# Kernel optimization log

Measured on AMD Instinct MI355X. Metric: run time of the kernel, lower is better.

Reference implementation:

```python
import jax, jax.numpy as jnp
import numpy as np

N = 32768          # tokens per modal
TOKEN_DIM = 1024
HID_DIM = 1024
SENSE_DIM = 256
K = 512            # centroids (shared size across modals)


def setup_inputs() -> dict:
    key = jax.random.key(0)
    ks = jax.random.split(key, 10)
    s = 0.02
    return {
        "text_emb": jax.random.normal(ks[0], (N, TOKEN_DIM), jnp.float32),
        "image_emb": jax.random.normal(ks[1], (N, TOKEN_DIM), jnp.float32),
        "text_W1": jax.random.normal(ks[2], (TOKEN_DIM, HID_DIM), jnp.float32) * s,
        "text_W2": jax.random.normal(ks[3], (HID_DIM, HID_DIM), jnp.float32) * s,
        "text_W3": jax.random.normal(ks[4], (HID_DIM, SENSE_DIM), jnp.float32) * s,
        "image_W1": jax.random.normal(ks[5], (TOKEN_DIM, HID_DIM), jnp.float32) * s,
        "image_W2": jax.random.normal(ks[6], (HID_DIM, HID_DIM), jnp.float32) * s,
        "image_W3": jax.random.normal(ks[7], (HID_DIM, SENSE_DIM), jnp.float32) * s,
        "centroids_raw": jax.random.uniform(ks[8], (K, SENSE_DIM), jnp.float32),
    }


def _sense_map(x, W1, W2, W3):
    # Linear(bias=False)+Tanh x3
    h = jnp.tanh(x @ W1)
    h = jnp.tanh(h @ W2)
    return jnp.tanh(h @ W3)  # [N, sense_dim]


def _assign(se, centroids):
    # squared distance [K, N] via expansion (same math as broadcast-subtract)
    c2 = jnp.sum(centroids * centroids, axis=1)[:, None]      # [K,1]
    e2 = jnp.sum(se * se, axis=1)[None, :]                     # [1,N]
    sqdist = c2 + e2 - 2.0 * (centroids @ se.T)                # [K,N]
    # torch argmax over (sqdist.T == min) picks first min -> argmin first occurrence
    return jnp.argmin(sqdist, axis=0)                          # [N] int


def reference(text_emb, image_emb, text_W1, text_W2, text_W3,
              image_W1, image_W2, image_W3, centroids_raw):
    centroids = jnp.tanh(centroids_raw)
    se_t = _sense_map(text_emb, text_W1, text_W2, text_W3)
    se_i = _sense_map(image_emb, image_W1, image_W2, image_W3)
    sc_t = _assign(se_t, centroids)
    sc_i = _assign(se_i, centroids)

    sense_embeddings = jnp.concatenate([se_t, se_i], axis=0)   # [2N, sense_dim]
    sense_class = jnp.concatenate([sc_t, sc_i], axis=0)        # [2N]
    word_class = jnp.concatenate([jnp.zeros((N,), jnp.int32),
                                  jnp.ones((N,), jnp.int32)])

    # ragged per-sense grouping represented jit-compatibly as a stable sort
    # permutation + per-sense counts (per modal)
    order_t = jnp.argsort(sc_t, stable=True)
    order_i = jnp.argsort(sc_i, stable=True)
    counts_t = jnp.zeros((K,), jnp.int32).at[sc_t].add(1)
    counts_i = jnp.zeros((K,), jnp.int32).at[sc_i].add(1)

    return (centroids, sense_embeddings, word_class, sense_class,
            order_t, counts_t, order_i, counts_i)
```

## Files before the change

### kernel.cpp

```cpp
#include <hip/hip_runtime.h>
#include <math.h>

#define NTOK 32768
typedef unsigned short ushort_t;

#define OFF_CENT 0
#define OFF_SE   131072
#define OFF_WC   16908288
#define OFF_SC   16973824
#define OFF_OT   17039360
#define OFF_CT   17072128
#define OFF_OI   17072640
#define OFF_CI   17105408

typedef __attribute__((ext_vector_type(8))) short short8v;
typedef __attribute__((ext_vector_type(4))) float f32x4;

__device__ __forceinline__ float dot4(float4 a, float4 b){
    return a.x*b.x + a.y*b.y + a.z*b.z + a.w*b.w;
}

__device__ __forceinline__ ushort_t f2bf(float x){
    unsigned int u = __float_as_uint(x);
    unsigned int r = (u + 0x7fffu + ((u >> 16) & 1u)) >> 16;
    return (ushort_t)r;
}
__device__ __forceinline__ float bf2f(ushort_t h){
    return __uint_as_float(((unsigned int)h) << 16);
}

__device__ __forceinline__ void gload16(const void* g, void* l){
    __builtin_amdgcn_global_load_lds(
        (const __attribute__((address_space(1))) void*)g,
        (__attribute__((address_space(3))) void*)l,
        16, 0, 0);
}

__device__ __forceinline__ void cvt8(float4 a, float4 b, short8v& h, short8v& l){
    float x[8] = {a.x, a.y, a.z, a.w, b.x, b.y, b.z, b.w};
    #pragma unroll
    for (int i = 0; i < 8; ++i) {
        ushort_t hh = f2bf(x[i]);
        h[i] = (short)hh;
        l[i] = (short)f2bf(x[i] - bf2f(hh));
    }
}

__global__ __launch_bounds__(64) void k_cent(const float* __restrict__ raw,
                                             float* __restrict__ out,
                                             float* __restrict__ c2,
                                             ushort_t* __restrict__ ch,
                                             ushort_t* __restrict__ cl)
{
    int c = blockIdx.x, l = threadIdx.x;
    float4 v = *(const float4*)(raw + (size_t)c*256 + l*4);
    float4 t;
    t.x = tanhf(v.x); t.y = tanhf(v.y); t.z = tanhf(v.z); t.w = tanhf(v.w);
    *(float4*)(out + OFF_CENT + (size_t)c*256 + l*4) = t;
    ushort4 h = make_ushort4(f2bf(t.x), f2bf(t.y), f2bf(t.z), f2bf(t.w));
    ushort4 lo = make_ushort4(f2bf(t.x - bf2f(h.x)), f2bf(t.y - bf2f(h.y)),
                              f2bf(t.z - bf2f(h.z)), f2bf(t.w - bf2f(h.w)));
    *(ushort4*)(ch + (size_t)c*256 + l*4) = h;
    *(ushort4*)(cl + (size_t)c*256 + l*4) = lo;
    float s = dot4(t, t);
    #pragma unroll
    for (int off = 32; off > 0; off >>= 1) s += __shfl_down(s, off);
    if (l == 0) c2[c] = s;
}

__global__ __launch_bounds__(256) void k_esplit(const float* __restrict__ x,
                                                ushort_t* __restrict__ hi,
                                                ushort_t* __restrict__ lo,
                                                long n4)
{
    long g = (long)blockIdx.x*256 + threadIdx.x;
    if (g >= n4) return;
    float4 v = ((const float4*)x)[g];
    ushort_t h0 = f2bf(v.x), h1 = f2bf(v.y), h2 = f2bf(v.z), h3 = f2bf(v.w);
    ushort4 h = make_ushort4(h0, h1, h2, h3);
    ushort4 l = make_ushort4(f2bf(v.x - bf2f(h0)), f2bf(v.y - bf2f(h1)),
                             f2bf(v.z - bf2f(h2)), f2bf(v.w - bf2f(h3)));
    ((ushort4*)hi)[g] = h;
    ((ushort4*)lo)[g] = l;
}

__device__ __forceinline__ void wsplit_tile(const float* __restrict__ W,
                                            ushort_t* __restrict__ Wt_hi,
                                            ushort_t* __restrict__ Wt_lo,
                                            int K, int N, int bx, int by)
{
    __shared__ float t[32][33];
    int k0 = by*32, n0 = bx*32;
    int tx = threadIdx.x & 31, ty = threadIdx.x >> 5;
    #pragma unroll
    for (int r = 0; r < 4; ++r)
        t[ty + r*8][tx] = W[(size_t)(k0 + ty + r*8)*N + n0 + tx];
    __syncthreads();
    #pragma unroll
    for (int r = 0; r < 4; ++r) {
        int n = ty + r*8;
        float x = t[tx][n];
        ushort_t h = f2bf(x);
        Wt_hi[(size_t)(n0+n)*K + k0 + tx] = h;
        Wt_lo[(size_t)(n0+n)*K + k0 + tx] = f2bf(x - bf2f(h));
    }
}

__global__ __launch_bounds__(256) void k_prep(
    const float* __restrict__ W1t, const float* __restrict__ W2t, const float* __restrict__ W3t,
    const float* __restrict__ W1i, const float* __restrict__ W2i, const float* __restrict__ W3i,
    ushort_t* __restrict__ wreg, float* __restrict__ out)
{
    const size_t WM = 4*1048576 + 2*262144;
    int b = blockIdx.x;
    if (b >= 4608) {
        int g = (b - 4608)*256 + threadIdx.x;
        float v = (g*4 < NTOK) ? 0.f : 1.f;
        ((float4*)(out + OFF_WC))[g] = make_float4(v, v, v, v);
        return;
    }
    int m = b / 2304;
    int r = b % 2304;
    ushort_t* base = wreg + (size_t)m*WM;
    const float* Ws[3][2] = {{W1t, W1i}, {W2t, W2i}, {W3t, W3i}};
    if (r < 1024) {
        wsplit_tile(Ws[0][m], base, base + 1048576, 1024, 1024, r % 32, r / 32);
    } else if (r < 2048) {
        int r2 = r - 1024;
        wsplit_tile(Ws[1][m], base + 2*1048576, base + 3*1048576, 1024, 1024, r2 % 32, r2 / 32);
    } else {
        int r3 = r - 2048;
        wsplit_tile(Ws[2][m], base + 4*1048576, base + 4*1048576 + 262144, 1024, 256, r3 % 8, r3 / 8);
    }
}

__global__ __launch_bounds__(512, 2) void k_gemm_l1(
    const float* __restrict__ Af, const ushort_t* __restrict__ Bt_hi,
    ushort_t* __restrict__ C_hi, ushort_t* __restrict__ C_lo,
    unsigned bDelta, int N)
{
    __shared__ ushort_t lds[65536];

    const int tid  = threadIdx.x;
    const int wave = tid >> 6, lane = tid & 63;
    const int wr = wave >> 2, wc = wave & 3;
    const int fr = lane & 15, fq = lane >> 4;

    int nwg = gridDim.x;
    int id = blockIdx.x;
    if (!(nwg & 7)) { int cpx = nwg >> 3; id = (id & 7)*cpx + (id >> 3); }
    const int nx = N >> 8;
    const int n0 = (id % nx) * 256;
    const int m0 = (id / nx) * 256;

    const int srow0 = tid >> 2;
    const int qx = (tid & 3) ^ ((srow0 >> 1) & 3);

    const float* fA0 = Af + (size_t)(m0 + srow0) * 1024 + qx*8;
    const float* fA1 = fA0 + 131072;
    const unsigned offB0 = (unsigned)(n0 + srow0) * 1024u + (unsigned)qx * 8u;
    const ushort_t* pB0  = Bt_hi + offB0;
    const ushort_t* pB1  = pB0 + 131072u;
    const ushort_t* pB0l = pB0 + bDelta;
    const ushort_t* pB1l = pB1 + bDelta;
    const unsigned ldsS0 = (unsigned)wave * 512u;
    const unsigned ldsS1 = ldsS0 + 4096u;
    const unsigned wOff  = ldsS0 + (unsigned)lane * 8u;

    const unsigned fb = (unsigned)fr*32u + (unsigned)((fq ^ ((fr >> 1) & 3)) * 8);
    const ushort_t* p0 = lds + fb;
    const ushort_t* p1 = p0 + 32768u;

    f32x4 acc[8][4] = {};

#define STGB(KT, WB) { \
    unsigned wb_ = (unsigned)(WB) * 32768u; \
    gload16(pB0  + (KT), lds + wb_ + 16384u + ldsS0); \
    gload16(pB1  + (KT), lds + wb_ + 16384u + ldsS1); \
    gload16(pB0l + (KT), lds + wb_ + 24576u + ldsS0); \
    gload16(pB1l + (KT), lds + wb_ + 24576u + ldsS1); \
}
#define RA1(P, hl, i) (*(const short8v*)((P) + (hl)*8192u + (unsigned)wr*4096u + (unsigned)(i)*512u))
#define RB1(P, hl, j) (*(const short8v*)((P) + 16384u + (hl)*8192u + (unsigned)wc*2048u + (unsigned)(j)*512u))
#define MM16(A8, B8, C4) __builtin_amdgcn_mfma_f32_16x16x32_bf16(A8, B8, C4, 0, 0, 0)

    {
        float4 a00 = *(const float4*)(fA0);
        float4 a01 = *(const float4*)(fA0 + 4);
        float4 a10 = *(const float4*)(fA1);
        float4 a11 = *(const float4*)(fA1 + 4);
        STGB(0, 0);
        short8v h0, l0, h1, l1;
        cvt8(a00, a01, h0, l0);
        cvt8(a10, a11, h1, l1);
        *(short8v*)(lds + wOff)          = h0;
        *(short8v*)(lds + 4096u + wOff)  = h1;
        *(short8v*)(lds + 8192u + wOff)  = l0;
        *(short8v*)(lds + 12288u + wOff) = l1;
    }
    __syncthreads();

    #pragma unroll 1
    for (int kt = 0; kt < 1024; kt += 32) {
        const int par = (kt >> 5) & 1;
        const ushort_t* cp = par ? p1 : p0;
        const bool pf = (kt + 32) < 1024;

        float4 a00, a01, a10, a11;
        if (pf) {
            a00 = *(const float4*)(fA0 + kt + 32);
            a01 = *(const float4*)(fA0 + kt + 36);
            a10 = *(const float4*)(fA1 + kt + 32);
            a11 = *(const float4*)(fA1 + kt + 36);
            STGB(kt + 32, par ^ 1);
        }

        short8v bh0 = RB1(cp,0,0), bl0 = RB1(cp,1,0);
        short8v bh1 = RB1(cp,0,1), bl1 = RB1(cp,1,1);
        short8v bh2 = RB1(cp,0,2), bl2 = RB1(cp,1,2);
        short8v bh3 = RB1(cp,0,3), bl3 = RB1(cp,1,3);

        __builtin_amdgcn_s_setprio(1);
        #pragma unroll
        for (int i = 0; i < 8; ++i) {
            short8v ah = RA1(cp,0,i), al = RA1(cp,1,i);
            acc[i][0] = MM16(ah, bh0, acc[i][0]);
            acc[i][1] = MM16(ah, bh1, acc[i][1]);
            acc[i][2] = MM16(ah, bh2, acc[i][2]);
            acc[i][3] = MM16(ah, bh3, acc[i][3]);
            acc[i][0] = MM16(ah, bl0, acc[i][0]);
            acc[i][1] = MM16(ah, bl1, acc[i][1]);
            acc[i][2] = MM16(ah, bl2, acc[i][2]);
            acc[i][3] = MM16(ah, bl3, acc[i][3]);
            acc[i][0] = MM16(al, bh0, acc[i][0]);
            acc[i][1] = MM16(al, bh1, acc[i][1]);
            acc[i][2] = MM16(al, bh2, acc[i][2]);
            acc[i][3] = MM16(al, bh3, acc[i][3]);
        }
        __builtin_amdgcn_s_setprio(0);

        if (pf) {
            unsigned wb = (unsigned)(par ^ 1) * 32768u;
            short8v h0, l0, h1, l1;
            cvt8(a00, a01, h0, l0);
            cvt8(a10, a11, h1, l1);
            *(short8v*)(lds + wb + wOff)          = h0;
            *(short8v*)(lds + wb + 4096u + wOff)  = h1;
            *(short8v*)(lds + wb + 8192u + wOff)  = l0;
            *(short8v*)(lds + wb + 12288u + wOff) = l1;
        }
        __syncthreads();
    }

    #pragma unroll
    for (int i = 0; i < 8; ++i)
        #pragma unroll
        for (int j = 0; j < 4; ++j)
            #pragma unroll
            for (int r = 0; r < 4; ++r) {
                int row = m0 + wr*128 + i*16 + fq*4 + r;
                int col = n0 + wc*64 + j*16 + fr;
                float t = tanhf(acc[i][j][r]);
                size_t idx = (size_t)row*N + col;
                ushort_t h = f2bf(t);
                C_hi[idx] = h;
                C_lo[idx] = f2bf(t - bf2f(h));
            }
#undef STGB
#undef RA1
#undef RB1
#undef MM16
}

__global__ __launch_bounds__(512, 2) void k_gemm_mfma256(
    const ushort_t* __restrict__ A_hi, const ushort_t* __restrict__ Bt_hi,
    ushort_t* __restrict__ C_hi, ushort_t* __restrict__ C_lo,
    unsigned aDelta, unsigned bDelta, int N)
{
    __shared__ ushort_t lds[65536];

    const int tid  = threadIdx.x;
    const int wave = tid >> 6, lane = tid & 63;
    const int wr = wave >> 2, wc = wave & 3;
    const int fr = lane & 15, fq = lane >> 4;

    int nwg = gridDim.x;
    int id = blockIdx.x;
    if (!(nwg & 7)) { int cpx = nwg >> 3; id = (id & 7)*cpx + (id >> 3); }
    const int nx = N >> 8;
    const int n0 = (id % nx) * 256;
    const int m0 = (id / nx) * 256;

    const int srow0 = tid >> 2;
    const int qx = (tid & 3) ^ ((srow0 >> 1) & 3);

    const unsigned offA0 = (unsigned)(m0 + srow0) * 1024u + (unsigned)qx * 8u;
    const unsigned offB0 = (unsigned)(n0 + srow0) * 1024u + (unsigned)qx * 8u;
    const ushort_t* pA0  = A_hi + offA0;
    const ushort_t* pA1  = pA0 + 131072u;
    const ushort_t* pA0l = pA0 + aDelta;
    const ushort_t* pA1l = pA1 + aDelta;
    const ushort_t* pB0  = Bt_hi + offB0;
    const ushort_t* pB1  = pB0 + 131072u;
    const ushort_t* pB0l = pB0 + bDelta;
    const ushort_t* pB1l = pB1 + bDelta;
    const unsigned ldsS0 = (unsigned)wave * 512u;
    const unsigned ldsS1 = ldsS0 + 4096u;

    const unsigned fb = (unsigned)fr*32u + (unsigned)((fq ^ ((fr >> 1) & 3)) * 8);
    const ushort_t* p0 = lds + fb;
    const ushort_t* p1 = p0 + 32768u;

    f32x4 acc[8][4] = {};

#define STG(KT, WB) { \
    unsigned wb_ = (unsigned)(WB) * 32768u; \
    gload16(pA0  + (KT), lds + wb_ +           ldsS0); \
    gload16(pA1  + (KT), lds + wb_ +           ldsS1); \
    gload16(pA0l + (KT), lds + wb_ +  8192u +  ldsS0); \
    gload16(pA1l + (KT), lds + wb_ +  8192u +  ldsS1); \
    gload16(pB0  + (KT), lds + wb_ + 16384u +  ldsS0); \
    gload16(pB1  + (KT), lds + wb_ + 16384u +  ldsS1); \
    gload16(pB0l + (KT), lds + wb_ + 24576u +  ldsS0); \
    gload16(pB1l + (KT), lds + wb_ + 24576u +  ldsS1); \
}
#define RA(P, hl, i) (*(const short8v*)((P) + (hl)*8192u + (unsigned)wr*4096u + (unsigned)(i)*512u))
#define RB(P, hl, j) (*(const short8v*)((P) + 16384u + (hl)*8192u + (unsigned)wc*2048u + (unsigned)(j)*512u))
#define MM16(A8, B8, C4) __builtin_amdgcn_mfma_f32_16x16x32_bf16(A8, B8, C4, 0, 0, 0)

    STG(0, 0);
    __syncthreads();

    #pragma unroll 1
    for (int kt = 0; kt < 1024; kt += 32) {
        const int par = (kt >> 5) & 1;
        const ushort_t* cp = par ? p1 : p0;

        short8v bh0 = RB(cp,0,0), bl0 = RB(cp,1,0);
        short8v bh1 = RB(cp,0,1), bl1 = RB(cp,1,1);
        short8v bh2 = RB(cp,0,2), bl2 = RB(cp,1,2);
        short8v bh3 = RB(cp,0,3), bl3 = RB(cp,1,3);

        if (kt + 32 < 1024) STG(kt + 32, par ^ 1);

        __builtin_amdgcn_s_setprio(1);
        #pragma unroll
        for (int i = 0; i < 8; ++i) {
            short8v ah = RA(cp,0,i), al = RA(cp,1,i);
            acc[i][0] = MM16(ah, bh0, acc[i][0]);
            acc[i][1] = MM16(ah, bh1, acc[i][1]);
            acc[i][2] = MM16(ah, bh2, acc[i][2]);
            acc[i][3] = MM16(ah, bh3, acc[i][3]);
            acc[i][0] = MM16(ah, bl0, acc[i][0]);
            acc[i][1] = MM16(ah, bl1, acc[i][1]);
            acc[i][2] = MM16(ah, bl2, acc[i][2]);
            acc[i][3] = MM16(ah, bl3, acc[i][3]);
            acc[i][0] = MM16(al, bh0, acc[i][0]);
            acc[i][1] = MM16(al, bh1, acc[i][1]);
            acc[i][2] = MM16(al, bh2, acc[i][2]);
            acc[i][3] = MM16(al, bh3, acc[i][3]);
        }
        __builtin_amdgcn_s_setprio(0);

        __syncthreads();
    }

    #pragma unroll
    for (int i = 0; i < 8; ++i)
        #pragma unroll
        for (int j = 0; j < 4; ++j)
            #pragma unroll
            for (int r = 0; r < 4; ++r) {
                int row = m0 + wr*128 + i*16 + fq*4 + r;
                int col = n0 + wc*64 + j*16 + fr;
                float t = tanhf(acc[i][j][r]);
                size_t idx = (size_t)row*N + col;
                ushort_t h = f2bf(t);
                C_hi[idx] = h;
                C_lo[idx] = f2bf(t - bf2f(h));
            }
#undef STG
#undef RA
#undef RB
#undef MM16
}

__global__ __launch_bounds__(256, 2) void k_gemm_mfma(
    const ushort_t* __restrict__ A_hi, const ushort_t* __restrict__ A_lo,
    const ushort_t* __restrict__ Bt_hi, const ushort_t* __restrict__ Bt_lo,
    ushort_t* __restrict__ C_hi, ushort_t* __restrict__ C_lo,
    float* __restrict__ Cf,
    int N)
{
    const int K = 1024;
    __shared__ ushort_t lds[16384];

    const int tid  = threadIdx.x;
    const int wave = tid >> 6, lane = tid & 63;
    const int wr = wave >> 1, wc = wave & 1;

    int nwg = gridDim.x * gridDim.y;
    int id = blockIdx.y * gridDim.x + blockIdx.x;
    if (!(nwg & 7)) { int cpx = nwg >> 3; id = (id & 7)*cpx + (id >> 3); }
    const int m0 = (id / gridDim.x) * 128, n0 = (id % gridDim.x) * 128;

    f32x4 acc[4][4] = {};

    int srow[2], sq[2], slbase[2];
    #pragma unroll
    for (int r = 0; r < 2; ++r) {
        int row = wave*32 + r*16 + (lane >> 2);
        srow[r]   = row;
        sq[r]     = (lane & 3) ^ ((row >> 1) & 3);
        slbase[r] = wave*1024 + r*512;
    }

    const int fr = lane & 15, fq = lane >> 4;

    for (int kt = 0; kt < K; kt += 32) {
        __syncthreads();
        #pragma unroll
        for (int r = 0; r < 2; ++r) {
            size_t ga = (size_t)(m0 + srow[r]) * K + kt + sq[r]*8;
            size_t gb = (size_t)(n0 + srow[r]) * K + kt + sq[r]*8;
            gload16(A_hi  + ga, lds          + slbase[r]);
            gload16(A_lo  + ga, lds + 4096   + slbase[r]);
            gload16(Bt_hi + gb, lds + 8192   + slbase[r]);
            gload16(Bt_lo + gb, lds + 12288  + slbase[r]);
        }
        __syncthreads();

        short8v ah[4], al[4], bh[4], bl[4];
        #pragma unroll
        for (int i = 0; i < 4; ++i) {
            int rowa = wr*64 + i*16 + fr;
            int offa = rowa*32 + ((fq ^ ((rowa >> 1) & 3)) * 8);
            ah[i] = *(const short8v*)(lds + offa);
            al[i] = *(const short8v*)(lds + 4096 + offa);
            int rowb = wc*64 + i*16 + fr;
            int offb = rowb*32 + ((fq ^ ((rowb >> 1) & 3)) * 8);
            bh[i] = *(const short8v*)(lds + 8192 + offb);
            bl[i] = *(const short8v*)(lds + 12288 + offb);
        }
        #pragma unroll
        for (int i = 0; i < 4; ++i)
            #pragma unroll
            for (int j = 0; j < 4; ++j) {
                acc[i][j] = __builtin_amdgcn_mfma_f32_16x16x32_bf16(ah[i], bh[j], acc[i][j], 0, 0, 0);
                acc[i][j] = __builtin_amdgcn_mfma_f32_16x16x32_bf16(ah[i], bl[j], acc[i][j], 0, 0, 0);
                acc[i][j] = __builtin_amdgcn_mfma_f32_16x16x32_bf16(al[i], bh[j], acc[i][j], 0, 0, 0);
            }
    }

    #pragma unroll
    for (int i = 0; i < 4; ++i)
        #pragma unroll
        for (int j = 0; j < 4; ++j)
            #pragma unroll
            for (int r = 0; r < 4; ++r) {
                int row = m0 + wr*64 + i*16 + fq*4 + r;
                int col = n0 + wc*64 + j*16 + fr;
                float t = tanhf(acc[i][j][r]);
                size_t idx = (size_t)row*N + col;
                if (Cf) Cf[idx] = t;
                if (C_hi) {
                    ushort_t h = f2bf(t);
                    C_hi[idx] = h;
                    C_lo[idx] = f2bf(t - bf2f(h));
                }
            }
}

__global__ __launch_bounds__(256) void k_assign_mfma(
    const ushort_t* __restrict__ SEh, const ushort_t* __restrict__ SEl,
    const ushort_t* __restrict__ ch, const ushort_t* __restrict__ cl,
    const float* __restrict__ c2,
    int* __restrict__ sc, float* __restrict__ out_w,
    int* __restrict__ blockHist)
{
    __shared__ ushort_t lds[16384];
    __shared__ float c2s[512];
    __shared__ float redD[128][2];
    __shared__ int   redI[128][2];

    const int modal = blockIdx.y;
    const int t0 = blockIdx.x * 128;
    const int tid  = threadIdx.x;
    const int wave = tid >> 6, lane = tid & 63;
    const int wr = wave >> 1, wc = wave & 1;
    const int fr = lane & 15, fq = lane >> 4;

    const ushort_t* seh = SEh + (size_t)modal * NTOK * 256;
    const ushort_t* sel = SEl + (size_t)modal * NTOK * 256;

    c2s[tid] = c2[tid];
    c2s[tid + 256] = c2[tid + 256];

    int srow[2], sq[2], slbase[2];
    #pragma unroll
    for (int r = 0; r < 2; ++r) {
        int row = wave*32 + r*16 + (lane >> 2);
        srow[r]   = row;
        sq[r]     = (lane & 3) ^ ((row >> 1) & 3);
        slbase[r] = wave*1024 + r*512;
    }

    float bd[16]; int bi[16];
    #pragma unroll
    for (int s = 0; s < 16; ++s) { bd[s] = 3.4e38f; bi[s] = 0; }

    for (int j = 0; j < 4; ++j) {
        f32x4 acc[4][4] = {};
        for (int kt = 0; kt < 256; kt += 32) {
            __syncthreads();
            #pragma unroll
            for (int r = 0; r < 2; ++r) {
                size_t ga = (size_t)(t0 + srow[r]) * 256 + kt + sq[r]*8;
                size_t gc = (size_t)(j*128 + srow[r]) * 256 + kt + sq[r]*8;
                gload16(seh + ga, lds          + slbase[r]);
                gload16(sel + ga, lds + 4096   + slbase[r]);
                gload16(ch  + gc, lds + 8192   + slbase[r]);
                gload16(cl  + gc, lds + 12288  + slbase[r]);
            }
// ... 208 lines not shown
    }
    classBase[modal*512 + c] = s[c] - total;
}

__global__ __launch_bounds__(256) void k_scatter(const int* __restrict__ sc,
                                                 const int* __restrict__ blockBase,
                                                 const int* __restrict__ classBase,
                                                 float* __restrict__ out)
{
    int modal = blockIdx.y, blk = blockIdx.x, tid = threadIdx.x;
    __shared__ int cls[256];
    int t = blk*256 + tid;
    int c = sc[modal*NTOK + t];
    cls[tid] = c;
    __syncthreads();
    int rank = 0;
    for (int j = 0; j < tid; ++j) rank += (cls[j] == c) ? 1 : 0;
    int pos = classBase[modal*512 + c] + blockBase[(modal*128 + blk)*512 + c] + rank;
    float* oo = out + (modal ? OFF_OI : OFF_OT);
    oo[pos] = (float)t;
}

extern "C" void kernel_launch(void* const* d_in, const int* in_sizes, int n_in,
                              void* d_out, int out_size, void* d_ws, size_t ws_size,
                              hipStream_t stream)
{
    const float* text_emb  = (const float*)d_in[0];
    const float* image_emb = (const float*)d_in[1];
    const float* W[2][3] = {
        {(const float*)d_in[2], (const float*)d_in[3], (const float*)d_in[4]},
        {(const float*)d_in[5], (const float*)d_in[6], (const float*)d_in[7]}
    };
    const float* cent_raw = (const float*)d_in[8];
    float* out = (float*)d_out;
    char* w = (char*)d_ws;

    int*   sc        = (int*)w;
    int*   blockHist = (int*)(w + 0x40000);
    int*   blockBase = (int*)(w + 0xC0000);
    int*   classBase = (int*)(w + 0x140000);
    float* c2        = (float*)(w + 0x141000);
    ushort_t* cent_h = (ushort_t*)(w + 0x142000);
    ushort_t* cent_l = (ushort_t*)(w + 0x182000);

    ushort_t* wreg = (ushort_t*)(w + 0x200000);
    const size_t WM = 4*1048576 + 2*262144;

    ushort_t* SEh = (ushort_t*)(w + 0x1400000);
    ushort_t* SEl = (ushort_t*)(w + 0x3400000);

    bool mfmaAssign = true;
    size_t actoff = 0x5400000;
    int Mc = 0;
    for (int c = NTOK; c >= 128; c >>= 1)
        if (actoff + (size_t)c*8192 <= ws_size) { Mc = c; break; }
    if (Mc == 0) {
        mfmaAssign = false;
        actoff = 0x1400000;
        for (int c = NTOK; c >= 128; c >>= 1)
            if (actoff + (size_t)c*8192 <= ws_size) { Mc = c; break; }
        if (Mc == 0) Mc = 128;
    }
    ushort_t* act = (ushort_t*)(w + actoff);
    const bool big = (Mc % 256 == 0);

    hipMemsetAsync(blockHist, 0, 2*128*512*sizeof(int), stream);

    k_cent<<<dim3(512), dim3(64), 0, stream>>>(cent_raw, out, c2, cent_h, cent_l);
    k_prep<<<dim3(4672), dim3(256), 0, stream>>>(
        W[0][0], W[0][1], W[0][2], W[1][0], W[1][1], W[1][2], wreg, out);

    for (int m = 0; m < 2; ++m) {
        const float* emb = m ? image_emb : text_emb;
        ushort_t* w1h = wreg + (size_t)m*WM;
        ushort_t* w1l = w1h + 1048576;
        ushort_t* w2h = w1l + 1048576;
        ushort_t* w2l = w2h + 1048576;
        ushort_t* w3h = w2l + 1048576;
        ushort_t* w3l = w3h + 262144;

        ushort_t* Ah = act;
        ushort_t* Al = Ah + (size_t)Mc*1024;
        ushort_t* Hh = Al + (size_t)Mc*1024;
        ushort_t* Hl = Hh + (size_t)Mc*1024;

        for (int s0 = 0; s0 < NTOK; s0 += Mc) {
            if (big) {
                k_gemm_l1<<<dim3((Mc/256)*4), dim3(512), 0, stream>>>(
                    emb + (size_t)s0*1024, w1h, Hh, Hl, 1048576u, 1024);
                k_gemm_mfma256<<<dim3((Mc/256)*4), dim3(512), 0, stream>>>(
                    Hh, w2h, Ah, Al, (unsigned)Mc*1024u, 1048576u, 1024);
            } else {
                long n4 = (long)Mc*1024/4;
                k_esplit<<<dim3((unsigned)((n4 + 255)/256)), dim3(256), 0, stream>>>(
                    emb + (size_t)s0*1024, Ah, Al, n4);
                k_gemm_mfma<<<dim3(8, Mc/128), dim3(256), 0, stream>>>(
                    Ah, Al, w1h, w1l, Hh, Hl, nullptr, 1024);
                k_gemm_mfma<<<dim3(8, Mc/128), dim3(256), 0, stream>>>(
                    Hh, Hl, w2h, w2l, Ah, Al, nullptr, 1024);
            }
            ushort_t* seh_ptr = mfmaAssign ? SEh + ((size_t)m*NTOK + s0)*256 : nullptr;
            ushort_t* sel_ptr = mfmaAssign ? SEl + ((size_t)m*NTOK + s0)*256 : nullptr;
            k_gemm_mfma<<<dim3(2, Mc/128), dim3(256), 0, stream>>>(
                Ah, Al, w3h, w3l, seh_ptr, sel_ptr,
                out + OFF_SE + ((size_t)m*NTOK + s0)*256, 256);
        }
    }

    if (mfmaAssign) {
        k_assign_mfma<<<dim3(256, 2), dim3(256), 0, stream>>>(
            SEh, SEl, cent_h, cent_l, c2, sc, out, blockHist);
    } else {
        k_assign<<<dim3(512, 2), dim3(256), 0, stream>>>(out, c2, sc, out, blockHist);
    }
    k_scan   <<<dim3(2),      dim3(512), 0, stream>>>(blockHist, blockBase, classBase, out);
    k_scatter<<<dim3(128, 2), dim3(256), 0, stream>>>(sc, blockBase, classBase, out);
}
```

Measured before the change: 1.042 ms.

## Use 32x32x16 MFMA with plane-blocked weight and hidden layouts for layers 1-2

Switches the two big GEMM kernels from 16x16x32 to 32x32x16 bf16 MFMA and stores the W1/W2 weights and the layer-1 output in a k-plane-blocked layout. Global-to-LDS copies become contiguous and match the fragment reads without XOR swizzling. The fallback path for chunk sizes below 256 is removed. The aim is fewer LDS reads per MFMA and cheaper addressing. The risk is more LDS bank conflicts from the unswizzled reads and scattered output stores in the layer-1 epilogue.

```diff
diff --git a/kernel.cpp b/kernel.cpp
--- a/kernel.cpp
+++ b/kernel.cpp
@@ -15,6 +15,11 @@
 
 typedef __attribute__((ext_vector_type(8))) short short8v;
 typedef __attribute__((ext_vector_type(4))) float f32x4;
+typedef __attribute__((ext_vector_type(16))) float f32x16;
+
+#define PLANE 2048
+#define KTBLK 8192
+#define RBLK  262144
 
 __device__ __forceinline__ float dot4(float4 a, float4 b){
     return a.x*b.x + a.y*b.y + a.z*b.z + a.w*b.w;
@@ -68,26 +73,36 @@
     if (l == 0) c2[c] = s;
 }
 
-__global__ __launch_bounds__(256) void k_esplit(const float* __restrict__ x,
-                                                ushort_t* __restrict__ hi,
-                                                ushort_t* __restrict__ lo,
-                                                long n4)
-{
-    long g = (long)blockIdx.x*256 + threadIdx.x;
-    if (g >= n4) return;
-    float4 v = ((const float4*)x)[g];
-    ushort_t h0 = f2bf(v.x), h1 = f2bf(v.y), h2 = f2bf(v.z), h3 = f2bf(v.w);
-    ushort4 h = make_ushort4(h0, h1, h2, h3);
-    ushort4 l = make_ushort4(f2bf(v.x - bf2f(h0)), f2bf(v.y - bf2f(h1)),
-                             f2bf(v.z - bf2f(h2)), f2bf(v.w - bf2f(h3)));
-    ((ushort4*)hi)[g] = h;
-    ((ushort4*)lo)[g] = l;
-}
-
-__device__ __forceinline__ void wsplit_tile(const float* __restrict__ W,
-                                            ushort_t* __restrict__ Wt_hi,
-                                            ushort_t* __restrict__ Wt_lo,
-                                            int K, int N, int bx, int by)
+__device__ __forceinline__ void wsplit_plane(const float* __restrict__ W,
+                                             ushort_t* __restrict__ Wt_hi,
+                                             ushort_t* __restrict__ Wt_lo,
+                                             int N, int bx, int by)
+{
+    __shared__ float t[32][33];
+    int k0 = by*32, n0 = bx*32;
+    int tx = threadIdx.x & 31, ty = threadIdx.x >> 5;
+    #pragma unroll
+    for (int r = 0; r < 4; ++r)
+        t[ty + r*8][tx] = W[(size_t)(k0 + ty + r*8)*N + n0 + tx];
+    __syncthreads();
+    const int kt = k0 >> 5;
+    const int s  = tx >> 3, e = tx & 7;
+    #pragma unroll
+    for (int r = 0; r < 4; ++r) {
+        int nl = ty + r*8;
+        int n = n0 + nl;
+        float x = t[tx][nl];
+        ushort_t h = f2bf(x);
+        size_t dst = (size_t)(n >> 8)*RBLK + (size_t)kt*KTBLK + s*PLANE + (n & 255)*8 + e;
+        Wt_hi[dst] = h;
+        Wt_lo[dst] = f2bf(x - bf2f(h));
+    }
+}
+
+__device__ __forceinline__ void wsplit_plain(const float* __restrict__ W,
+                                             ushort_t* __restrict__ Wt_hi,
+                                             ushort_t* __restrict__ Wt_lo,
+                                             int K, int N, int bx, int by)
 {
     __shared__ float t[32][33];
     int k0 = by*32, n0 = bx*32;
@@ -124,86 +139,114 @@
     ushort_t* base = wreg + (size_t)m*WM;
     const float* Ws[3][2] = {{W1t, W1i}, {W2t, W2i}, {W3t, W3i}};
     if (r < 1024) {
-        wsplit_tile(Ws[0][m], base, base + 1048576, 1024, 1024, r % 32, r / 32);
+        wsplit_plane(Ws[0][m], base, base + 1048576, 1024, r % 32, r / 32);
     } else if (r < 2048) {
         int r2 = r - 1024;
-        wsplit_tile(Ws[1][m], base + 2*1048576, base + 3*1048576, 1024, 1024, r2 % 32, r2 / 32);
+        wsplit_plane(Ws[1][m], base + 2*1048576, base + 3*1048576, 1024, r2 % 32, r2 / 32);
     } else {
         int r3 = r - 2048;
-        wsplit_tile(Ws[2][m], base + 4*1048576, base + 4*1048576 + 262144, 1024, 256, r3 % 8, r3 / 8);
-    }
+        wsplit_plain(Ws[2][m], base + 4*1048576, base + 4*1048576 + 262144, 1024, 256, r3 % 8, r3 / 8);
+    }
+}
+
+#define MM32(A8, B8, C16) __builtin_amdgcn_mfma_f32_32x32x16_bf16(A8, B8, C16, 0, 0, 0)
+
+#define RAP(P, hl, kk, i) (*(const short8v*)((P) + (hl)*8192u + (kk)*4096u + (unsigned)(i)*256u))
+#define RBP(P, hl, kk, j) (*(const short8v*)((P) + 16384u + (hl)*8192u + (kk)*4096u + (unsigned)(j)*256u))
+
+#define MFMA_TILE(PA, PB) { \
+    short8v b000 = RBP(PB,0,0,0), b001 = RBP(PB,1,0,0); \
+    short8v b010 = RBP(PB,0,1,0), b011 = RBP(PB,1,1,0); \
+    short8v b100 = RBP(PB,0,0,1), b101 = RBP(PB,1,0,1); \
+    short8v b110 = RBP(PB,0,1,1), b111 = RBP(PB,1,1,1); \
+    __builtin_amdgcn_s_setprio(1); \
+    _Pragma("unroll") \
+    for (int i = 0; i < 4; ++i) { \
+        short8v ah0 = RAP(PA,0,0,i), al0 = RAP(PA,1,0,i); \
+        short8v ah1 = RAP(PA,0,1,i), al1 = RAP(PA,1,1,i); \
+        acc[i][0] = MM32(ah0, b000, acc[i][0]); \
+        acc[i][1] = MM32(ah0, b100, acc[i][1]); \
+        acc[i][0] = MM32(ah0, b001, acc[i][0]); \
+        acc[i][1] = MM32(ah0, b101, acc[i][1]); \
+        acc[i][0] = MM32(al0, b000, acc[i][0]); \
+        acc[i][1] = MM32(al0, b100, acc[i][1]); \
+        acc[i][0] = MM32(ah1, b010, acc[i][0]); \
+        acc[i][1] = MM32(ah1, b110, acc[i][1]); \
+        acc[i][0] = MM32(ah1, b011, acc[i][0]); \
+        acc[i][1] = MM32(ah1, b111, acc[i][1]); \
+        acc[i][0] = MM32(al1, b010, acc[i][0]); \
+        acc[i][1] = MM32(al1, b110, acc[i][1]); \
+    } \
+    __builtin_amdgcn_s_setprio(0); \
 }
 
 __global__ __launch_bounds__(512, 2) void k_gemm_l1(
-    const float* __restrict__ Af, const ushort_t* __restrict__ Bt_hi,
+    const float* __restrict__ Af, const ushort_t* __restrict__ Btp,
     ushort_t* __restrict__ C_hi, ushort_t* __restrict__ C_lo,
-    unsigned bDelta, int N)
+    unsigned bDelta)
 {
     __shared__ ushort_t lds[65536];
 
     const int tid  = threadIdx.x;
     const int wave = tid >> 6, lane = tid & 63;
     const int wr = wave >> 2, wc = wave & 3;
-    const int fr = lane & 15, fq = lane >> 4;
+    const int l31 = lane & 31, lk = lane >> 5;
 
     int nwg = gridDim.x;
     int id = blockIdx.x;
     if (!(nwg & 7)) { int cpx = nwg >> 3; id = (id & 7)*cpx + (id >> 3); }
-    const int nx = N >> 8;
-    const int n0 = (id % nx) * 256;
-    const int m0 = (id / nx) * 256;
-
-    const int srow0 = tid >> 2;
-    const int qx = (tid & 3) ^ ((srow0 >> 1) & 3);
-
-    const float* fA0 = Af + (size_t)(m0 + srow0) * 1024 + qx*8;
+    const int n0 = (id & 3) * 256;
+    const int m0 = (id >> 2) * 256;
+
+    const int q  = tid & 3;
+    const int sr = tid >> 2;
+    const float* fA0 = Af + (size_t)(m0 + sr) * 1024 + q*8;
     const float* fA1 = fA0 + 131072;
-    const unsigned offB0 = (unsigned)(n0 + srow0) * 1024u + (unsigned)qx * 8u;
-    const ushort_t* pB0  = Bt_hi + offB0;
-    const ushort_t* pB1  = pB0 + 131072u;
+    const unsigned aw0 = (unsigned)q*PLANE + (unsigned)sr*8u;
+    const unsigned aw1 = aw0 + 1024u;
+
+    const ushort_t* pB0 = Btp + (size_t)(n0 >> 8)*RBLK + wave*512 + lane*8;
     const ushort_t* pB0l = pB0 + bDelta;
-    const ushort_t* pB1l = pB1 + bDelta;
-    const unsigned ldsS0 = (unsigned)wave * 512u;
-    const unsigned ldsS1 = ldsS0 + 4096u;
-    const unsigned wOff  = ldsS0 + (unsigned)lane * 8u;
-
-    const unsigned fb = (unsigned)fr*32u + (unsigned)((fq ^ ((fr >> 1) & 3)) * 8);
-    const ushort_t* p0 = lds + fb;
-    const ushort_t* p1 = p0 + 32768u;
-
-    f32x4 acc[8][4] = {};
-
-#define STGB(KT, WB) { \
+    const unsigned ldsB0 = 16384u + (unsigned)wave*512u;
+
+    const unsigned fbu = (unsigned)lk*PLANE + (unsigned)l31*8u;
+    const ushort_t* pA = lds + fbu + (unsigned)wr*1024u;
+    const ushort_t* pB = lds + fbu + (unsigned)wc*512u;
+    const ushort_t* pA1b = pA + 32768u;
+    const ushort_t* pB1b = pB + 32768u;
+
+    f32x16 acc[4][2] = {};
+
+#define STGB1(KT, WB) { \
     unsigned wb_ = (unsigned)(WB) * 32768u; \
-    gload16(pB0  + (KT), lds + wb_ + 16384u + ldsS0); \
-    gload16(pB1  + (KT), lds + wb_ + 16384u + ldsS1); \
-    gload16(pB0l + (KT), lds + wb_ + 24576u + ldsS0); \
-    gload16(pB1l + (KT), lds + wb_ + 24576u + ldsS1); \
-}
-#define RA1(P, hl, i) (*(const short8v*)((P) + (hl)*8192u + (unsigned)wr*4096u + (unsigned)(i)*512u))
-#define RB1(P, hl, j) (*(const short8v*)((P) + 16384u + (hl)*8192u + (unsigned)wc*2048u + (unsigned)(j)*512u))
-#define MM16(A8, B8, C4) __builtin_amdgcn_mfma_f32_16x16x32_bf16(A8, B8, C4, 0, 0, 0)
+    unsigned ko = (unsigned)(KT) * 256u; \
+    gload16(pB0  + ko,        lds + wb_ + ldsB0); \
+    gload16(pB0  + ko + 4096, lds + wb_ + ldsB0 + 4096u); \
+    gload16(pB0l + ko,        lds + wb_ + 8192u + ldsB0); \
+    gload16(pB0l + ko + 4096, lds + wb_ + 8192u + ldsB0 + 4096u); \
+}
 
     {
         float4 a00 = *(const float4*)(fA0);
         float4 a01 = *(const float4*)(fA0 + 4);
         float4 a10 = *(const float4*)(fA1);
         float4 a11 = *(const float4*)(fA1 + 4);
-        STGB(0, 0);
+        STGB1(0, 0);
         short8v h0, l0, h1, l1;
         cvt8(a00, a01, h0, l0);
         cvt8(a10, a11, h1, l1);
-        *(short8v*)(lds + wOff)          = h0;
-        *(short8v*)(lds + 4096u + wOff)  = h1;
-        *(short8v*)(lds + 8192u + wOff)  = l0;
-        *(short8v*)(lds + 12288u + wOff) = l1;
+        *(short8v*)(lds + aw0)          = h0;
+        *(short8v*)(lds + aw1)          = h1;
+        *(short8v*)(lds + 8192u + aw0)  = l0;
+        *(short8v*)(lds + 8192u + aw1)  = l1;
     }
     __syncthreads();
 
     #pragma unroll 1
     for (int kt = 0; kt < 1024; kt += 32) {
         const int par = (kt >> 5) & 1;
-        const ushort_t* cp = par ? p1 : p0;
+        const ushort_t* cpA = par ? pA1b : pA;
+        const ushort_t* cpB = par ? pB1b : pB;
         const bool pf = (kt + 32) < 1024;
 
         float4 a00, a01, a10, a11;
@@ -212,177 +255,119 @@
             a01 = *(const float4*)(fA0 + kt + 36);
             a10 = *(const float4*)(fA1 + kt + 32);
             a11 = *(const float4*)(fA1 + kt + 36);
-            STGB(kt + 32, par ^ 1);
-        }
-
-        short8v bh0 = RB1(cp,0,0), bl0 = RB1(cp,1,0);
-        short8v bh1 = RB1(cp,0,1), bl1 = RB1(cp,1,1);
-        short8v bh2 = RB1(cp,0,2), bl2 = RB1(cp,1,2);
-        short8v bh3 = RB1(cp,0,3), bl3 = RB1(cp,1,3);
-
-        __builtin_amdgcn_s_setprio(1);
-        #pragma unroll
-        for (int i = 0; i < 8; ++i) {
-            short8v ah = RA1(cp,0,i), al = RA1(cp,1,i);
-            acc[i][0] = MM16(ah, bh0, acc[i][0]);
-            acc[i][1] = MM16(ah, bh1, acc[i][1]);
-            acc[i][2] = MM16(ah, bh2, acc[i][2]);
-            acc[i][3] = MM16(ah, bh3, acc[i][3]);
-            acc[i][0] = MM16(ah, bl0, acc[i][0]);
-            acc[i][1] = MM16(ah, bl1, acc[i][1]);
-            acc[i][2] = MM16(ah, bl2, acc[i][2]);
-            acc[i][3] = MM16(ah, bl3, acc[i][3]);
-            acc[i][0] = MM16(al, bh0, acc[i][0]);
-            acc[i][1] = MM16(al, bh1, acc[i][1]);
-            acc[i][2] = MM16(al, bh2, acc[i][2]);
-            acc[i][3] = MM16(al, bh3, acc[i][3]);
-        }
-        __builtin_amdgcn_s_setprio(0);
+            STGB1(kt + 32, par ^ 1);
+        }
+
+        MFMA_TILE(cpA, cpB)
 
         if (pf) {
             unsigned wb = (unsigned)(par ^ 1) * 32768u;
             short8v h0, l0, h1, l1;
             cvt8(a00, a01, h0, l0);
             cvt8(a10, a11, h1, l1);
-            *(short8v*)(lds + wb + wOff)          = h0;
-            *(short8v*)(lds + wb + 4096u + wOff)  = h1;
-            *(short8v*)(lds + wb + 8192u + wOff)  = l0;
-            *(short8v*)(lds + wb + 12288u + wOff) = l1;
+            *(short8v*)(lds + wb + aw0)          = h0;
+            *(short8v*)(lds + wb + aw1)          = h1;
+            *(short8v*)(lds + wb + 8192u + aw0)  = l0;
+            *(short8v*)(lds + wb + 8192u + aw1)  = l1;
         }
         __syncthreads();
     }
 
     #pragma unroll
-    for (int i = 0; i < 8; ++i)
-        #pragma unroll
-        for (int j = 0; j < 4; ++j)
-            #pragma unroll
-            for (int r = 0; r < 4; ++r) {
-                int row = m0 + wr*128 + i*16 + fq*4 + r;
-                int col = n0 + wc*64 + j*16 + fr;
+    for (int i = 0; i < 4; ++i)
+        #pragma unroll
+        for (int j = 0; j < 2; ++j)
+            #pragma unroll
+            for (int r = 0; r < 16; ++r) {
+                int row = m0 + wr*128 + i*32 + (r & 3) + 8*(r >> 2) + 4*lk;
+                int col = n0 + wc*64 + j*32 + l31;
                 float t = tanhf(acc[i][j][r]);
-                size_t idx = (size_t)row*N + col;
+                size_t idx = (size_t)(row >> 8)*RBLK + (size_t)(col >> 5)*KTBLK
+                           + ((col >> 3) & 3)*PLANE + (row & 255)*8 + (col & 7);
                 ushort_t h = f2bf(t);
                 C_hi[idx] = h;
                 C_lo[idx] = f2bf(t - bf2f(h));
             }
-#undef STGB
-#undef RA1
-#undef RB1
-#undef MM16
-}
-
-__global__ __launch_bounds__(512, 2) void k_gemm_mfma256(
-    const ushort_t* __restrict__ A_hi, const ushort_t* __restrict__ Bt_hi,
+#undef STGB1
+}
+
+__global__ __launch_bounds__(512, 2) void k_gemm_l2(
+    const ushort_t* __restrict__ Ap, const ushort_t* __restrict__ Btp,
     ushort_t* __restrict__ C_hi, ushort_t* __restrict__ C_lo,
-    unsigned aDelta, unsigned bDelta, int N)
+    unsigned aDelta, unsigned bDelta)
 {
     __shared__ ushort_t lds[65536];
 
     const int tid  = threadIdx.x;
     const int wave = tid >> 6, lane = tid & 63;
     const int wr = wave >> 2, wc = wave & 3;
-    const int fr = lane & 15, fq = lane >> 4;
+    const int l31 = lane & 31, lk = lane >> 5;
 
     int nwg = gridDim.x;
     int id = blockIdx.x;
     if (!(nwg & 7)) { int cpx = nwg >> 3; id = (id & 7)*cpx + (id >> 3); }
-    const int nx = N >> 8;
-    const int n0 = (id % nx) * 256;
-    const int m0 = (id / nx) * 256;
-
-    const int srow0 = tid >> 2;
-    const int qx = (tid & 3) ^ ((srow0 >> 1) & 3);
-
-    const unsigned offA0 = (unsigned)(m0 + srow0) * 1024u + (unsigned)qx * 8u;
-    const unsigned offB0 = (unsigned)(n0 + srow0) * 1024u + (unsigned)qx * 8u;
-    const ushort_t* pA0  = A_hi + offA0;
-    const ushort_t* pA1  = pA0 + 131072u;
+    const int n0 = (id & 3) * 256;
+    const int m0 = (id >> 2) * 256;
+
+    const ushort_t* pA0 = Ap  + (size_t)(m0 >> 8)*RBLK + wave*512 + lane*8;
     const ushort_t* pA0l = pA0 + aDelta;
-    const ushort_t* pA1l = pA1 + aDelta;
-    const ushort_t* pB0  = Bt_hi + offB0;
-    const ushort_t* pB1  = pB0 + 131072u;
+    const ushort_t* pB0 = Btp + (size_t)(n0 >> 8)*RBLK + wave*512 + lane*8;
     const ushort_t* pB0l = pB0 + bDelta;
-    const ushort_t* pB1l = pB1 + bDelta;
-    const unsigned ldsS0 = (unsigned)wave * 512u;
-    const unsigned ldsS1 = ldsS0 + 4096u;
-
-    const unsigned fb = (unsigned)fr*32u + (unsigned)((fq ^ ((fr >> 1) & 3)) * 8);
-    const ushort_t* p0 = lds + fb;
-    const ushort_t* p1 = p0 + 32768u;
-
-    f32x4 acc[8][4] = {};
-
-#define STG(KT, WB) { \
+    const unsigned ldsA0 = (unsigned)wave*512u;
+    const unsigned ldsB0 = 16384u + (unsigned)wave*512u;
+
+    const unsigned fbu = (unsigned)lk*PLANE + (unsigned)l31*8u;
+    const ushort_t* pA = lds + fbu + (unsigned)wr*1024u;
+    const ushort_t* pB = lds + fbu + (unsigned)wc*512u;
+    const ushort_t* pA1b = pA + 32768u;
+    const ushort_t* pB1b = pB + 32768u;
+
+    f32x16 acc[4][2] = {};
+
+#define STG2(KT, WB) { \
     unsigned wb_ = (unsigned)(WB) * 32768u; \
-    gload16(pA0  + (KT), lds + wb_ +           ldsS0); \
-    gload16(pA1  + (KT), lds + wb_ +           ldsS1); \
-    gload16(pA0l + (KT), lds + wb_ +  8192u +  ldsS0); \
-    gload16(pA1l + (KT), lds + wb_ +  8192u +  ldsS1); \
-    gload16(pB0  + (KT), lds + wb_ + 16384u +  ldsS0); \
-    gload16(pB1  + (KT), lds + wb_ + 16384u +  ldsS1); \
-    gload16(pB0l + (KT), lds + wb_ + 24576u +  ldsS0); \
-    gload16(pB1l + (KT), lds + wb_ + 24576u +  ldsS1); \
-}
-#define RA(P, hl, i) (*(const short8v*)((P) + (hl)*8192u + (unsigned)wr*4096u + (unsigned)(i)*512u))
-#define RB(P, hl, j) (*(const short8v*)((P) + 16384u + (hl)*8192u + (unsigned)wc*2048u + (unsigned)(j)*512u))
-#define MM16(A8, B8, C4) __builtin_amdgcn_mfma_f32_16x16x32_bf16(A8, B8, C4, 0, 0, 0)
-
-    STG(0, 0);
+    unsigned ko = (unsigned)(KT) * 256u; \
+    gload16(pA0  + ko,        lds + wb_ + ldsA0); \
+    gload16(pA0  + ko + 4096, lds + wb_ + ldsA0 + 4096u); \
+    gload16(pA0l + ko,        lds + wb_ + 8192u + ldsA0); \
+    gload16(pA0l + ko + 4096, lds + wb_ + 8192u + ldsA0 + 4096u); \
+    gload16(pB0  + ko,        lds + wb_ + ldsB0); \
+    gload16(pB0  + ko + 4096, lds + wb_ + ldsB0 + 4096u); \
+    gload16(pB0l + ko,        lds + wb_ + 8192u + ldsB0); \
+    gload16(pB0l + ko + 4096, lds + wb_ + 8192u + ldsB0 + 4096u); \
+}
+
+    STG2(0, 0);
     __syncthreads();
 
     #pragma unroll 1
     for (int kt = 0; kt < 1024; kt += 32) {
         const int par = (kt >> 5) & 1;
-        const ushort_t* cp = par ? p1 : p0;
-
-        short8v bh0 = RB(cp,0,0), bl0 = RB(cp,1,0);
-        short8v bh1 = RB(cp,0,1), bl1 = RB(cp,1,1);
-        short8v bh2 = RB(cp,0,2), bl2 = RB(cp,1,2);
-        short8v bh3 = RB(cp,0,3), bl3 = RB(cp,1,3);
-
-        if (kt + 32 < 1024) STG(kt + 32, par ^ 1);
-
-        __builtin_amdgcn_s_setprio(1);
-        #pragma unroll
-        for (int i = 0; i < 8; ++i) {
-            short8v ah = RA(cp,0,i), al = RA(cp,1,i);
-            acc[i][0] = MM16(ah, bh0, acc[i][0]);
-            acc[i][1] = MM16(ah, bh1, acc[i][1]);
-            acc[i][2] = MM16(ah, bh2, acc[i][2]);
-            acc[i][3] = MM16(ah, bh3, acc[i][3]);
-            acc[i][0] = MM16(ah, bl0, acc[i][0]);
-            acc[i][1] = MM16(ah, bl1, acc[i][1]);
-            acc[i][2] = MM16(ah, bl2, acc[i][2]);
-            acc[i][3] = MM16(ah, bl3, acc[i][3]);
-            acc[i][0] = MM16(al, bh0, acc[i][0]);
-            acc[i][1] = MM16(al, bh1, acc[i][1]);
-            acc[i][2] = MM16(al, bh2, acc[i][2]);
-            acc[i][3] = MM16(al, bh3, acc[i][3]);
-        }
-        __builtin_amdgcn_s_setprio(0);
+        const ushort_t* cpA = par ? pA1b : pA;
+        const ushort_t* cpB = par ? pB1b : pB;
+
+        if (kt + 32 < 1024) STG2(kt + 32, par ^ 1);
+
+        MFMA_TILE(cpA, cpB)
 
         __syncthreads();
     }
 
     #pragma unroll
-    for (int i = 0; i < 8; ++i)
-        #pragma unroll
-        for (int j = 0; j < 4; ++j)
-            #pragma unroll
-            for (int r = 0; r < 4; ++r) {
-                int row = m0 + wr*128 + i*16 + fq*4 + r;
-                int col = n0 + wc*64 + j*16 + fr;
+    for (int i = 0; i < 4; ++i)
+        #pragma unroll
+        for (int j = 0; j < 2; ++j)
+            #pragma unroll
+            for (int r = 0; r < 16; ++r) {
+                int row = m0 + wr*128 + i*32 + (r & 3) + 8*(r >> 2) + 4*lk;
+                int col = n0 + wc*64 + j*32 + l31;
                 float t = tanhf(acc[i][j][r]);
-                size_t idx = (size_t)row*N + col;
+                size_t idx = (size_t)row*1024 + col;
                 ushort_t h = f2bf(t);
                 C_hi[idx] = h;
                 C_lo[idx] = f2bf(t - bf2f(h));
             }
-#undef STG
-#undef RA
-#undef RB
-#undef MM16
+#undef STG2
 }
 
 __global__ __launch_bounds__(256, 2) void k_gemm_mfma(
@@ -783,17 +768,16 @@
     bool mfmaAssign = true;
     size_t actoff = 0x5400000;
     int Mc = 0;
-    for (int c = NTOK; c >= 128; c >>= 1)
+    for (int c = NTOK; c >= 256; c >>= 1)
         if (actoff + (size_t)c*8192 <= ws_size) { Mc = c; break; }
     if (Mc == 0) {
         mfmaAssign = false;
         actoff = 0x1400000;
-        for (int c = NTOK; c >= 128; c >>= 1)
+        for (int c = NTOK; c >= 256; c >>= 1)
             if (actoff + (size_t)c*8192 <= ws_size) { Mc = c; break; }
-        if (Mc == 0) Mc = 128;
+        if (Mc == 0) Mc = 256;
     }
     ushort_t* act = (ushort_t*)(w + actoff);
-    const bool big = (Mc % 256 == 0);
 
     hipMemsetAsync(blockHist, 0, 2*128*512*sizeof(int), stream);
 
@@ -804,10 +788,8 @@
     for (int m = 0; m < 2; ++m) {
         const float* emb = m ? image_emb : text_emb;
         ushort_t* w1h = wreg + (size_t)m*WM;
-        ushort_t* w1l = w1h + 1048576;
-        ushort_t* w2h = w1l + 1048576;
-        ushort_t* w2l = w2h + 1048576;
-        ushort_t* w3h = w2l + 1048576;
+        ushort_t* w2h = w1h + 2*1048576;
+        ushort_t* w3h = w1h + 4*1048576;
         ushort_t* w3l = w3h + 262144;
 
         ushort_t* Ah = act;
@@ -816,20 +798,10 @@
         ushort_t* Hl = Hh + (size_t)Mc*1024;
 
         for (int s0 = 0; s0 < NTOK; s0 += Mc) {
-            if (big) {
-                k_gemm_l1<<<dim3((Mc/256)*4), dim3(512), 0, stream>>>(
-                    emb + (size_t)s0*1024, w1h, Hh, Hl, 1048576u, 1024);
-                k_gemm_mfma256<<<dim3((Mc/256)*4), dim3(512), 0, stream>>>(
-                    Hh, w2h, Ah, Al, (unsigned)Mc*1024u, 1048576u, 1024);
-            } else {
-                long n4 = (long)Mc*1024/4;
-                k_esplit<<<dim3((unsigned)((n4 + 255)/256)), dim3(256), 0, stream>>>(
-                    emb + (size_t)s0*1024, Ah, Al, n4);
-                k_gemm_mfma<<<dim3(8, Mc/128), dim3(256), 0, stream>>>(
-                    Ah, Al, w1h, w1l, Hh, Hl, nullptr, 1024);
-                k_gemm_mfma<<<dim3(8, Mc/128), dim3(256), 0, stream>>>(
-                    Hh, Hl, w2h, w2l, Ah, Al, nullptr, 1024);
-            }
+            k_gemm_l1<<<dim3((Mc/256)*4), dim3(512), 0, stream>>>(
+                emb + (size_t)s0*1024, w1h, Hh, Hl, 1048576u);
+            k_gemm_l2<<<dim3((Mc/256)*4), dim3(512), 0, stream>>>(
+                Hh, w2h, Ah, Al, (unsigned)Mc*1024u, 1048576u);
             ushort_t* seh_ptr = mfmaAssign ? SEh + ((size_t)m*NTOK + s0)*256 : nullptr;
             ushort_t* sel_ptr = mfmaAssign ? SEl + ((size_t)m*NTOK + s0)*256 : nullptr;
             k_gemm_mfma<<<dim3(2, Mc/128), dim3(256), 0, stream>>>(
```

New measurement: 1.120 ms. 7.5% more time.

## Double-buffer LDS in generic MFMA GEMM and drop small-chunk fallback path

Applied to the files above, without the earlier changes.

Rewrites the k_gemm_mfma main loop so the LDS tile is double-buffered. The next k-slice is prefetched while MFMAs run on the current one, and one barrier per iteration replaces two. Address math is hoisted into precomputed pointers, and MFMA priority is raised during the compute phase. It also removes the non-256-multiple chunk fallback path, always using the specialized layer-1/2 kernels, and doubles LDS use for the kernel, which may lower occupancy.

```diff
diff --git a/kernel.cpp b/kernel.cpp
--- a/kernel.cpp
+++ b/kernel.cpp
@@ -392,64 +392,85 @@
     float* __restrict__ Cf,
     int N)
 {
-    const int K = 1024;
-    __shared__ ushort_t lds[16384];
+    __shared__ ushort_t lds[32768];
 
     const int tid  = threadIdx.x;
     const int wave = tid >> 6, lane = tid & 63;
     const int wr = wave >> 1, wc = wave & 1;
+    const int fr = lane & 15, fq = lane >> 4;
 
     int nwg = gridDim.x * gridDim.y;
     int id = blockIdx.y * gridDim.x + blockIdx.x;
     if (!(nwg & 7)) { int cpx = nwg >> 3; id = (id & 7)*cpx + (id >> 3); }
     const int m0 = (id / gridDim.x) * 128, n0 = (id % gridDim.x) * 128;
 
+    const int sl = lane >> 2;
+    const int sq = (lane & 3) ^ ((sl >> 1) & 3);
+    const unsigned ga0 = (unsigned)(m0 + wave*32 + sl) * 1024u + (unsigned)sq * 8u;
+    const unsigned gb0 = (unsigned)(n0 + wave*32 + sl) * 1024u + (unsigned)sq * 8u;
+    const ushort_t* pa0 = A_hi  + ga0;       const ushort_t* pa1 = pa0 + 16384u;
+    const ushort_t* pal0 = A_lo + ga0;       const ushort_t* pal1 = pal0 + 16384u;
+    const ushort_t* pb0 = Bt_hi + gb0;       const ushort_t* pb1 = pb0 + 16384u;
+    const ushort_t* pbl0 = Bt_lo + gb0;      const ushort_t* pbl1 = pbl0 + 16384u;
+    const unsigned sl0 = (unsigned)wave * 1024u;
+    const unsigned sl1 = sl0 + 512u;
+
+    const unsigned fb = (unsigned)fr*32u + (unsigned)((fq ^ ((fr >> 1) & 3)) * 8);
+    const ushort_t* q0 = lds + fb;
+    const ushort_t* q1 = q0 + 16384u;
+
     f32x4 acc[4][4] = {};
 
-    int srow[2], sq[2], slbase[2];
-    #pragma unroll
-    for (int r = 0; r < 2; ++r) {
-        int row = wave*32 + r*16 + (lane >> 2);
-        srow[r]   = row;
-        sq[r]     = (lane & 3) ^ ((row >> 1) & 3);
-        slbase[r] = wave*1024 + r*512;
-    }
-
-    const int fr = lane & 15, fq = lane >> 4;
-
-    for (int kt = 0; kt < K; kt += 32) {
+#define STG3(KT, WB) { \
+    unsigned wb_ = (unsigned)(WB) * 16384u; \
+    gload16(pa0  + (KT), lds + wb_ +           sl0); \
+    gload16(pa1  + (KT), lds + wb_ +           sl1); \
+    gload16(pal0 + (KT), lds + wb_ +  4096u +  sl0); \
+    gload16(pal1 + (KT), lds + wb_ +  4096u +  sl1); \
+    gload16(pb0  + (KT), lds + wb_ +  8192u +  sl0); \
+    gload16(pb1  + (KT), lds + wb_ +  8192u +  sl1); \
+    gload16(pbl0 + (KT), lds + wb_ + 12288u +  sl0); \
+    gload16(pbl1 + (KT), lds + wb_ + 12288u +  sl1); \
+}
+#define RA3(P, hl, i) (*(const short8v*)((P) + (hl)*4096u + (unsigned)wr*2048u + (unsigned)(i)*512u))
+#define RB3(P, hl, j) (*(const short8v*)((P) + 8192u + (hl)*4096u + (unsigned)wc*2048u + (unsigned)(j)*512u))
+#define MM16(A8, B8, C4) __builtin_amdgcn_mfma_f32_16x16x32_bf16(A8, B8, C4, 0, 0, 0)
+
+    STG3(0, 0);
+    __syncthreads();
+
+    #pragma unroll 1
+    for (int kt = 0; kt < 1024; kt += 32) {
+        const int par = (kt >> 5) & 1;
+        const ushort_t* cp = par ? q1 : q0;
+
+        short8v bh0 = RB3(cp,0,0), bl0 = RB3(cp,1,0);
+        short8v bh1 = RB3(cp,0,1), bl1 = RB3(cp,1,1);
+        short8v bh2 = RB3(cp,0,2), bl2 = RB3(cp,1,2);
+        short8v bh3 = RB3(cp,0,3), bl3 = RB3(cp,1,3);
+
+        if (kt + 32 < 1024) STG3(kt + 32, par ^ 1);
+
+        __builtin_amdgcn_s_setprio(1);
+        #pragma unroll
+        for (int i = 0; i < 4; ++i) {
+            short8v ah = RA3(cp,0,i), al = RA3(cp,1,i);
+            acc[i][0] = MM16(ah, bh0, acc[i][0]);
+            acc[i][1] = MM16(ah, bh1, acc[i][1]);
+            acc[i][2] = MM16(ah, bh2, acc[i][2]);
+            acc[i][3] = MM16(ah, bh3, acc[i][3]);
+            acc[i][0] = MM16(ah, bl0, acc[i][0]);
+            acc[i][1] = MM16(ah, bl1, acc[i][1]);
+            acc[i][2] = MM16(ah, bl2, acc[i][2]);
+            acc[i][3] = MM16(ah, bl3, acc[i][3]);
+            acc[i][0] = MM16(al, bh0, acc[i][0]);
+            acc[i][1] = MM16(al, bh1, acc[i][1]);
+            acc[i][2] = MM16(al, bh2, acc[i][2]);
+            acc[i][3] = MM16(al, bh3, acc[i][3]);
+        }
+        __builtin_amdgcn_s_setprio(0);
+
         __syncthreads();
-        #pragma unroll
-        for (int r = 0; r < 2; ++r) {
-            size_t ga = (size_t)(m0 + srow[r]) * K + kt + sq[r]*8;
-            size_t gb = (size_t)(n0 + srow[r]) * K + kt + sq[r]*8;
-            gload16(A_hi  + ga, lds          + slbase[r]);
-            gload16(A_lo  + ga, lds + 4096   + slbase[r]);
-            gload16(Bt_hi + gb, lds + 8192   + slbase[r]);
-            gload16(Bt_lo + gb, lds + 12288  + slbase[r]);
-        }
-        __syncthreads();
-
-        short8v ah[4], al[4], bh[4], bl[4];
-        #pragma unroll
-        for (int i = 0; i < 4; ++i) {
-            int rowa = wr*64 + i*16 + fr;
-            int offa = rowa*32 + ((fq ^ ((rowa >> 1) & 3)) * 8);
-            ah[i] = *(const short8v*)(lds + offa);
-            al[i] = *(const short8v*)(lds + 4096 + offa);
-            int rowb = wc*64 + i*16 + fr;
-            int offb = rowb*32 + ((fq ^ ((rowb >> 1) & 3)) * 8);
-            bh[i] = *(const short8v*)(lds + 8192 + offb);
-            bl[i] = *(const short8v*)(lds + 12288 + offb);
-        }
-        #pragma unroll
-        for (int i = 0; i < 4; ++i)
-            #pragma unroll
-            for (int j = 0; j < 4; ++j) {
-                acc[i][j] = __builtin_amdgcn_mfma_f32_16x16x32_bf16(ah[i], bh[j], acc[i][j], 0, 0, 0);
-                acc[i][j] = __builtin_amdgcn_mfma_f32_16x16x32_bf16(ah[i], bl[j], acc[i][j], 0, 0, 0);
-                acc[i][j] = __builtin_amdgcn_mfma_f32_16x16x32_bf16(al[i], bh[j], acc[i][j], 0, 0, 0);
-            }
     }
 
     #pragma unroll
@@ -469,6 +490,10 @@
                     C_lo[idx] = f2bf(t - bf2f(h));
                 }
             }
+#undef STG3
+#undef RA3
+#undef RB3
+#undef MM16
 }
 
 __global__ __launch_bounds__(256) void k_assign_mfma(
@@ -783,17 +808,16 @@
     bool mfmaAssign = true;
     size_t actoff = 0x5400000;
     int Mc = 0;
-    for (int c = NTOK; c >= 128; c >>= 1)
+    for (int c = NTOK; c >= 256; c >>= 1)
         if (actoff + (size_t)c*8192 <= ws_size) { Mc = c; break; }
     if (Mc == 0) {
         mfmaAssign = false;
         actoff = 0x1400000;
-        for (int c = NTOK; c >= 128; c >>= 1)
+        for (int c = NTOK; c >= 256; c >>= 1)
             if (actoff + (size_t)c*8192 <= ws_size) { Mc = c; break; }
-        if (Mc == 0) Mc = 128;
+        if (Mc == 0) Mc = 256;
     }
     ushort_t* act = (ushort_t*)(w + actoff);
-    const bool big = (Mc % 256 == 0);
 
     hipMemsetAsync(blockHist, 0, 2*128*512*sizeof(int), stream);
 
@@ -804,10 +828,8 @@
     for (int m = 0; m < 2; ++m) {
         const float* emb = m ? image_emb : text_emb;
         ushort_t* w1h = wreg + (size_t)m*WM;
-        ushort_t* w1l = w1h + 1048576;
-        ushort_t* w2h = w1l + 1048576;
-        ushort_t* w2l = w2h + 1048576;
-        ushort_t* w3h = w2l + 1048576;
+        ushort_t* w2h = w1h + 2*1048576;
+        ushort_t* w3h = w1h + 4*1048576;
         ushort_t* w3l = w3h + 262144;
 
         ushort_t* Ah = act;
@@ -816,20 +838,10 @@
         ushort_t* Hl = Hh + (size_t)Mc*1024;
 
         for (int s0 = 0; s0 < NTOK; s0 += Mc) {
-            if (big) {
-                k_gemm_l1<<<dim3((Mc/256)*4), dim3(512), 0, stream>>>(
-                    emb + (size_t)s0*1024, w1h, Hh, Hl, 1048576u, 1024);
-                k_gemm_mfma256<<<dim3((Mc/256)*4), dim3(512), 0, stream>>>(
-                    Hh, w2h, Ah, Al, (unsigned)Mc*1024u, 1048576u, 1024);
-            } else {
-                long n4 = (long)Mc*1024/4;
-                k_esplit<<<dim3((unsigned)((n4 + 255)/256)), dim3(256), 0, stream>>>(
-                    emb + (size_t)s0*1024, Ah, Al, n4);
-                k_gemm_mfma<<<dim3(8, Mc/128), dim3(256), 0, stream>>>(
-                    Ah, Al, w1h, w1l, Hh, Hl, nullptr, 1024);
-                k_gemm_mfma<<<dim3(8, Mc/128), dim3(256), 0, stream>>>(
-                    Hh, Hl, w2h, w2l, Ah, Al, nullptr, 1024);
-            }
+            k_gemm_l1<<<dim3((Mc/256)*4), dim3(512), 0, stream>>>(
+                emb + (size_t)s0*1024, w1h, Hh, Hl, 1048576u, 1024);
+            k_gemm_mfma256<<<dim3((Mc/256)*4), dim3(512), 0, stream>>>(
+                Hh, w2h, Ah, Al, (unsigned)Mc*1024u, 1048576u, 1024);
             ushort_t* seh_ptr = mfmaAssign ? SEh + ((size_t)m*NTOK + s0)*256 : nullptr;
             ushort_t* sel_ptr = mfmaAssign ? SEl + ((size_t)m*NTOK + s0)*256 : nullptr;
             k_gemm_mfma<<<dim3(2, Mc/128), dim3(256), 0, stream>>>(
```

Result: no change. 1.030 ms (-1.1%).
